# Kernel optimization log

Measured on AMD Instinct MI355X. Metric: run time of the kernel, lower is better.

Reference implementation:

```python
import jax, jax.numpy as jnp
import numpy as np

HEADS = 8
DIM_KEY = 64
DIM_VALUE = 192
DIM = 1536
NRPF = 192  # num_rel_pos_features, divisible by 6
SEQ = DIM_VALUE * HEADS  # 1536; source code reshapes with n = dim_value*heads as seq len
BATCH = 4


def get_positional_embed(seq_len, feature_size):
    # distances: (2*seq_len - 1,)
    distances = jnp.arange(-seq_len + 1, seq_len, dtype=jnp.float32)
    absd = jnp.abs(distances)[:, None]
    nb = feature_size // 6  # num_basis_per_class (3 fns * 2 for sign)
    # exponential
    max_range = np.log(seq_len) / np.log(2.0)
    half_life = 2.0 ** jnp.linspace(3.0, max_range, nb)
    pe_exp = jnp.exp(-jnp.log(2.0) / half_life[None, :] * absd)
    # central mask
    center_widths = 2.0 ** jnp.arange(1, nb + 1, dtype=jnp.float32) - 1.0
    pe_cm = (center_widths[None, :] > absd).astype(jnp.float32)
    # gamma
    stddev = seq_len / (2.0 * nb)
    start_mean = seq_len / nb
    mean = jnp.linspace(start_mean, float(seq_len), nb)[None, :]
    concentration = (mean / stddev) ** 2
    rate = mean / (stddev ** 2)
    log_unnorm = jax.scipy.special.xlogy(concentration - 1.0, absd) - rate * absd
    log_norm = jax.scipy.special.gammaln(concentration) - concentration * jnp.log(rate)
    probs = jnp.exp(log_unnorm - log_norm) + 1e-8
    pe_g = probs / jnp.max(probs, axis=-1, keepdims=True)
    emb = jnp.concatenate([pe_exp, pe_cm, pe_g], axis=-1)  # (2n-1, feature_size/2)
    return jnp.concatenate([emb, jnp.sign(distances)[:, None] * emb], axis=-1)


def relative_shift(x):
    # x: (b, h, t1, t2) with t2 = 2*t1 - 1 -> (b, h, t1, t1)
    b, h, t1, t2 = x.shape
    x = jnp.pad(x, ((0, 0), (0, 0), (0, 0), (1, 0)))  # (b,h,t1,t2+1)
    x = x.reshape(b, h, t2 + 1, t1)[:, :, 1:, :].reshape(b, h, t1, t2)
    return x[..., : (t2 + 2) // 2]


def setup_inputs() -> dict:
    key = jax.random.key(0)
    ks = jax.random.split(key, 9)
    s = 0.02
    return {
        "x": jax.random.normal(ks[0], (BATCH, SEQ, DIM), jnp.float32),
        "Wq": jax.random.normal(ks[1], (DIM, DIM_KEY * HEADS), jnp.float32) * s,
        "Wk": jax.random.normal(ks[2], (DIM, DIM_KEY * HEADS), jnp.float32) * s,
        "Wv": jax.random.normal(ks[3], (DIM, DIM_VALUE * HEADS), jnp.float32) * s,
        "Wrel": jax.random.normal(ks[4], (NRPF, DIM_KEY * HEADS), jnp.float32) * s,
        "rel_content_bias": jax.random.normal(ks[5], (1, HEADS, 1, DIM_KEY), jnp.float32),
        "rel_pos_bias": jax.random.normal(ks[6], (1, HEADS, 1, DIM_KEY), jnp.float32),
        "Wout": jax.random.normal(ks[7], (DIM_VALUE * HEADS, DIM), jnp.float32) * s,
        "b_out": jnp.zeros((DIM,), jnp.float32),
    }


def reference(x, Wq, Wk, Wv, Wrel, rel_content_bias, rel_pos_bias, Wout, b_out):
    b, n, _ = x.shape
    h, dk, dv = HEADS, DIM_KEY, DIM_VALUE
    scale = dk ** -0.5
    q = (x @ Wq).reshape(b, n, h, dk).transpose(0, 2, 1, 3) * scale  # (b,h,n,dk)
    k = (x @ Wk).reshape(b, n, h, dk).transpose(0, 2, 1, 3)
    v = (x @ Wv).reshape(b, n, h, dv).transpose(0, 2, 1, 3)
    content_logits = jnp.einsum('bhid,bhjd->bhij', q + rel_content_bias, k)
    positions = get_positional_embed(n, NRPF)  # (2n-1, NRPF)
    rel_k = (positions @ Wrel).reshape(2 * n - 1, h, dk).transpose(1, 0, 2)  # (h,2n-1,dk)
    rel_logits = jnp.einsum('bhid,hjd->bhij', q + rel_pos_bias, rel_k)  # (b,h,n,2n-1)
    rel_logits = relative_shift(rel_logits)  # (b,h,n,n)
    attn = jax.nn.softmax(content_logits + rel_logits, axis=-1)
    out = jnp.einsum('bhij,bhjd->bhid', attn, v)  # (b,h,n,dv)
    out = out.transpose(0, 2, 1, 3).reshape(b, n, h * dv)
    return out @ Wout + b_out
```

## Files before the change

kernel.cpp:

```cpp
#include <hip/hip_runtime.h>
#include <cmath>

#define B_SZ    4
#define N_SEQ   1536
#define D_MODEL 1536
#define H_N     8
#define DK      64
#define DV      192
#define HDK     512
#define HDV     1536
#define NRPF    192
#define NB      32
#define NREL    3071
#define QKS     2560
#define SM_BASE 12.0f

typedef unsigned short u16;
typedef __attribute__((ext_vector_type(8))) short short8;
typedef __attribute__((ext_vector_type(4))) float f32x4;

#define MFMA_B16(a, b, c) __builtin_amdgcn_mfma_f32_16x16x32_bf16(a, b, c, 0, 0, 0)

__device__ __forceinline__ float bf2f(u16 u) {
    union { unsigned u; float f; } x; x.u = ((unsigned)u) << 16; return x.f;
}
__device__ __forceinline__ u16 f2bf(float f) {
    union { float f; unsigned u; } x; x.f = f;
    unsigned r = x.u + 0x7FFFu + ((x.u >> 16) & 1u);
    return (u16)(r >> 16);
}
__device__ __forceinline__ void gload16(const u16* g, u16* l) {
    __builtin_amdgcn_global_load_lds(
        (const __attribute__((address_space(1))) unsigned int*)(const void*)g,
        (__attribute__((address_space(3))) unsigned int*)(void*)l, 16, 0, 0);
}

__global__ __launch_bounds__(256) void prep_kernel(
    const float* __restrict__ x,
    const float* __restrict__ Wq, const float* __restrict__ Wk,
    const float* __restrict__ Wv, const float* __restrict__ Wout,
    const float* __restrict__ Wrel,
    u16* __restrict__ posb, u16* __restrict__ xb,
    u16* __restrict__ wqkvt, u16* __restrict__ woutt, u16* __restrict__ wrelt) {
    const int z = blockIdx.z;
    const int tid = threadIdx.x;
    if (z < 5) {
        const float* W; u16* Wt; int K, N; float scale = 1.0f;
        if (z == 0)      { W = Wq;   Wt = wqkvt;                        K = 1536; N = 512;  scale = 0.125f; }
        else if (z == 1) { W = Wk;   Wt = wqkvt + (size_t)512 * 1536;   K = 1536; N = 512;  }
        else if (z == 2) { W = Wv;   Wt = wqkvt + (size_t)1024 * 1536;  K = 1536; N = 1536; }
        else if (z == 3) { W = Wout; Wt = woutt;                        K = 1536; N = 1536; }
        else             { W = Wrel; Wt = wrelt;                        K = 192;  N = 512;  }
        __shared__ float tile[32][33];
        int n0 = blockIdx.x * 32, k0 = blockIdx.y * 32;
        if (n0 >= N || k0 >= K) return;
        int tx = tid & 31, ty = tid >> 5;
        for (int r = ty; r < 32; r += 8) tile[r][tx] = W[(size_t)(k0 + r) * N + n0 + tx];
        __syncthreads();
        for (int r = ty; r < 32; r += 8)
            Wt[(size_t)(n0 + r) * K + k0 + tx] = f2bf(tile[tx][r] * scale);
    } else if (z == 5) {
        const int r = blockIdx.y * 64 + blockIdx.x;
        const int j = tid;
        if (r >= NREL) {
            if (j < 96) {
                posb[(size_t)r * NRPF + j] = 0;
                posb[(size_t)r * NRPF + 96 + j] = 0;
            }
            return;
        }
        __shared__ float gprobs[NB];
        float dist = (float)(r - (N_SEQ - 1));
        float absd = fabsf(dist);
        int cls = j >> 5, jj = j & 31;
        float val = 0.0f;
        if (j < 96) {
            if (cls == 0) {
                const float max_range = 10.584962500721156f;
                float hl = exp2f(3.0f + (float)jj * (max_range - 3.0f) / 31.0f);
                val = expf(-0.6931471805599453f / hl * absd);
            } else if (cls == 1) {
                float cw = exp2f((float)(jj + 1)) - 1.0f;
                val = (cw > absd) ? 1.0f : 0.0f;
            } else {
                float mean = 48.0f + (float)jj * (1536.0f - 48.0f) / 31.0f;
                float conc = (mean / 24.0f) * (mean / 24.0f);
                float rate = mean / 576.0f;
                float lu = (conc - 1.0f) * logf(absd) - rate * absd;
                float ln = lgammaf(conc) - conc * logf(rate);
                float prob = expf(lu - ln) + 1e-8f;
                gprobs[jj] = prob;
                val = prob;
            }
        }
        __syncthreads();
        if (j < 96) {
            if (cls == 2) {
                float mx = gprobs[0];
                #pragma unroll
                for (int t = 1; t < NB; ++t) mx = fmaxf(mx, gprobs[t]);
                val = val / mx;
            }
            float sgn = (dist > 0.f) ? 1.f : ((dist < 0.f) ? -1.f : 0.f);
            posb[(size_t)r * NRPF + j]      = f2bf(val);
            posb[(size_t)r * NRPF + 96 + j] = f2bf(sgn * val);
        }
    } else {
        const int n8 = (B_SZ * N_SEQ) * D_MODEL / 8;
        const float4* p = (const float4*)x;
        for (int i = (blockIdx.y * 64 + blockIdx.x) * 256 + tid; i < n8; i += 64 * 48 * 256) {
            float4 a = p[i * 2], bq = p[i * 2 + 1];
            short8 o;
            o[0] = (short)f2bf(a.x);  o[1] = (short)f2bf(a.y);
            o[2] = (short)f2bf(a.z);  o[3] = (short)f2bf(a.w);
            o[4] = (short)f2bf(bq.x); o[5] = (short)f2bf(bq.y);
            o[6] = (short)f2bf(bq.z); o[7] = (short)f2bf(bq.w);
            *(short8*)(xb + (size_t)i * 8) = o;
        }
    }
}

#define BM 128
#define BN 128
#define BK 64
__device__ __forceinline__ void gemm_body(
    const u16* __restrict__ A, const u16* __restrict__ Bt,
    u16* __restrict__ Cb, float* __restrict__ Cf,
    const float* __restrict__ bias, int Mstore, int N, int K) {
    __shared__ u16 sA[BM * BK] __attribute__((aligned(16)));
    __shared__ u16 sB[BN * BK] __attribute__((aligned(16)));
    const int tid  = threadIdx.x;
    const int lane = tid & 63;
    const int w    = tid >> 6;
    const int wm   = w >> 1, wn = w & 1;
    const int row0 = blockIdx.y * BM, col0 = blockIdx.x * BN;

    f32x4 acc[4][4];
    #pragma unroll
    for (int i = 0; i < 4; ++i)
        #pragma unroll
        for (int j = 0; j < 4; ++j) acc[i][j] = (f32x4){0.f, 0.f, 0.f, 0.f};

    int srow[4], soff[4];
    #pragma unroll
    for (int i = 0; i < 4; ++i) {
        const int ci = i * 256 + tid;
        const int r  = ci >> 3;
        const int lc = (ci & 7) ^ (r & 7);
        srow[i] = r;
        soff[i] = lc * 8;
    }

    for (int kt = 0; kt < K; kt += BK) {
        #pragma unroll
        for (int i = 0; i < 4; ++i) {
            gload16(A + (size_t)(row0 + srow[i]) * K + kt + soff[i],
                    sA + (i * 256 + w * 64) * 8);
            gload16(Bt + (size_t)(col0 + srow[i]) * K + kt + soff[i],
                    sB + (i * 256 + w * 64) * 8);
        }
        __syncthreads();
        short8 af[2][4], bg[2][4];
        #pragma unroll
        for (int s = 0; s < 2; ++s) {
            #pragma unroll
            for (int mi = 0; mi < 4; ++mi) {
                const int rr = wm * 64 + mi * 16 + (lane & 15);
                af[s][mi] = *(const short8*)&sA[rr * 64 + (((s * 4 + (lane >> 4)) ^ (rr & 7)) * 8)];
            }
            #pragma unroll
            for (int ni = 0; ni < 4; ++ni) {
                const int rr = wn * 64 + ni * 16 + (lane & 15);
                bg[s][ni] = *(const short8*)&sB[rr * 64 + (((s * 4 + (lane >> 4)) ^ (rr & 7)) * 8)];
            }
        }
        #pragma unroll
        for (int s = 0; s < 2; ++s)
            #pragma unroll
            for (int mi = 0; mi < 4; ++mi)
                #pragma unroll
                for (int ni = 0; ni < 4; ++ni)
                    acc[mi][ni] = MFMA_B16(af[s][mi], bg[s][ni], acc[mi][ni]);
        __syncthreads();
    }
    const int rb = (lane >> 4) * 4;
    const int cl = lane & 15;
    #pragma unroll
    for (int mi = 0; mi < 4; ++mi) {
        #pragma unroll
        for (int r = 0; r < 4; ++r) {
            const int gr = row0 + wm * 64 + mi * 16 + rb + r;
            if (gr >= Mstore) continue;
            #pragma unroll
            for (int ni = 0; ni < 4; ++ni) {
                const int gc = col0 + wn * 64 + ni * 16 + cl;
                float v = acc[mi][ni][r];
                if (bias) v += bias[gc];
                if (Cb) Cb[(size_t)gr * N + gc] = f2bf(v);
                else    Cf[(size_t)gr * N + gc] = v;
            }
        }
    }
}

__global__ __launch_bounds__(256) void gemm_bf16(
    const u16* __restrict__ A, const u16* __restrict__ Bt,
    u16* __restrict__ Cb, float* __restrict__ Cf,
    const float* __restrict__ bias, int Mstore, int N, int K) {
    gemm_body(A, Bt, Cb, Cf, bias, Mstore, N, K);
}

__global__ __launch_bounds__(256) void gemm_qkv_rel(
    const u16* __restrict__ xb, const u16* __restrict__ wqkvt, u16* __restrict__ qkvb,
    const u16* __restrict__ posb, const u16* __restrict__ wrelt, u16* __restrict__ relkb) {
    if (blockIdx.z == 0) {
        gemm_body(xb, wqkvt, qkvb, nullptr, nullptr, B_SZ * N_SEQ, QKS, D_MODEL);
    } else {
        if (blockIdx.y * BM >= 3072 || blockIdx.x * BN >= HDK) return;
        gemm_body(posb, wrelt, relkb, nullptr, nullptr, 3072, HDK, NRPF);
    }
}

__global__ __launch_bounds__(256) void transpose_v(const u16* __restrict__ qkv,
                                                   u16* __restrict__ vt) {
    __shared__ u16 tile[64][72];
    int nt = blockIdx.x, ct = blockIdx.y, bh = blockIdx.z;
    int b = bh >> 3, h = bh & 7;
    int tid = threadIdx.x;
    for (int t = tid; t < 512; t += 256) {
        int r = t >> 3, ch = t & 7;
        short8 v = *(const short8*)(qkv + ((size_t)(b * N_SEQ + nt * 64 + r)) * QKS
                                        + 1024 + h * DV + ct * 64 + ch * 8);
        #pragma unroll
        for (int e = 0; e < 8; ++e) tile[ch * 8 + e][r] = (u16)v[e];
    }
    __syncthreads();
    for (int t = tid; t < 512; t += 256) {
        int c = t >> 3, ch = t & 7;
        short8 v;
        #pragma unroll
        for (int e = 0; e < 8; ++e) v[e] = (short)tile[c][ch * 8 + e];
        *(short8*)(vt + ((size_t)((b * 8 + h) * DV + ct * 64 + c)) * N_SEQ
                      + nt * 64 + ch * 8) = v;
    }
}

__global__ __launch_bounds__(256, 3) void attn_mfma(
    const u16* __restrict__ qb, const u16* __restrict__ kb,
    const u16* __restrict__ vtb, const u16* __restrict__ relkb,
    const float* __restrict__ cbias, const float* __restrict__ pbias,
    u16* __restrict__ att) {
    __shared__ u16 sK[2 * 64 * 64] __attribute__((aligned(16)));
    __shared__ u16 sP[64 * 64] __attribute__((aligned(16)));
    __shared__ u16 sRW[192 * 64] __attribute__((aligned(16)));
    __shared__ float sL[64];

    const int tid  = threadIdx.x;
    const int lane = tid & 63;
    const int w    = tid >> 6;
    const int h    = blockIdx.x & 7;
    const int q9   = blockIdx.x >> 3;
    const int b    = q9 / 24;
    const int i0   = (q9 % 24) * 64;
    const int rbase0 = (N_SEQ - 64) - i0;

    const int c15 = lane & 15;
    const int g   = lane >> 4;
    const int g4  = g << 2;
    const int arow = w * 16 + c15;
    const int growb = w * 16 + g4;

    for (int t = tid; t < 512; t += 256) {
        const int row = t >> 3, ch = t & 7;
        short8 v = *(const short8*)(qb + ((size_t)(b * N_SEQ + i0 + row)) * QKS
                                       + h * DK + ch * 8);
        short8 c8, p8;
        #pragma unroll
        for (int e = 0; e < 8; ++e) {
            float f = bf2f((u16)v[e]);
            c8[e] = (short)f2bf(f + cbias[h * DK + ch * 8 + e]);
            p8[e] = (short)f2bf(f + pbias[h * DK + ch * 8 + e]);
        }
        const int dst = row * 64 + ((ch ^ (row & 7)) * 8);
        *(short8*)&sK[dst] = c8;
        *(short8*)&sP[dst] = p8;
    }
    __syncthreads();

    short8 aqc[2], aqp[2];
    #pragma unroll
    for (int s = 0; s < 2; ++s) {
        const int off = arow * 64 + (((s * 4 + g) ^ (arow & 7)) * 8);
        aqc[s] = *(const short8*)&sK[off];
        aqp[s] = *(const short8*)&sP[off];
    }
    __syncthreads();

    auto stage_k = [&](int j0s, int buf) {
        #pragma unroll
        for (int i = 0; i < 2; ++i) {
            const int ci = i * 256 + tid, row = ci >> 3;
            const int sch = ((ci & 7) ^ (row & 7)) * 8;
            gload16(kb + ((size_t)(b * N_SEQ + j0s + row)) * QKS + h * DK + sch,
                    sK + buf * 4096 + ci * 8);
        }
    };
    auto stage_r = [&](int lr0) {
        const int pw0 = lr0 % 192;
        #pragma unroll
        for (int i = 0; i < 2; ++i) {
            const int ci = i * 256 + tid, row = ci >> 3;
            const int sch = ((ci & 7) ^ ((pw0 + row) & 7)) * 8;
            gload16(relkb + ((size_t)(rbase0 + lr0 + row)) * HDK + h * DK + sch,
                    sRW + pw0 * 64 + ci * 8);
        }
    };

    stage_k(0, 0);
    stage_r(0);
    stage_r(64);
    asm volatile("s_waitcnt vmcnt(0) lgkmcnt(0)" ::: "memory");
    __builtin_amdgcn_sched_barrier(0);
    __builtin_amdgcn_s_barrier();

    f32x4 O[12];
    #pragma unroll
    for (int i = 0; i < 12; ++i) O[i] = (f32x4){0.f, 0.f, 0.f, 0.f};
    float L[4] = {0.f, 0.f, 0.f, 0.f};

    for (int jt = 0; jt < 24; ++jt) {
        const int j0 = jt * 64;
        if (jt < 23) {
            stage_k(j0 + 64, (jt + 1) & 1);
            stage_r(j0 + 128);
        }
        f32x4 S[4], G5[5];
        #pragma unroll
        for (int f = 0; f < 4; ++f) S[f] = (f32x4){0.f, 0.f, 0.f, 0.f};
        #pragma unroll
        for (int t = 0; t < 5; ++t) G5[t] = (f32x4){0.f, 0.f, 0.f, 0.f};
        const int kbase = (jt & 1) * 4096;
        const int ph = (jt % 3) * 64;
        #pragma unroll
        for (int s = 0; s < 2; ++s) {
            short8 kf[4], rf[5];
            #pragma unroll
            for (int f = 0; f < 4; ++f) {
                const int br = f * 16 + c15;
                kf[f] = *(const short8*)&sK[kbase + br * 64 + (((s * 4 + g) ^ (br & 7)) * 8)];
            }
            #pragma unroll
            for (int t = 0; t < 5; ++t) {
                int lrb = ph + (3 - w + t) * 16;
                if (lrb >= 192) lrb -= 192;
                const int pr = lrb + c15;
                rf[t] = *(const short8*)&sRW[pr * 64 + (((s * 4 + g) ^ (pr & 7)) * 8)];
            }
            #pragma unroll
            for (int f = 0; f < 4; ++f) S[f] = MFMA_B16(aqc[s], kf[f], S[f]);
            #pragma unroll
            for (int t = 0; t < 5; ++t) G5[t] = MFMA_B16(aqp[s], rf[t], G5[t]);
        }
        #pragma unroll
        for (int r = 0; r < 4; ++r) {
            const int src = (lane & 48) | ((c15 + 15 - g4 - r) & 15);
            const float rot0 = __shfl(G5[0][r], src, 64);
            const float rot1 = __shfl(G5[1][r], src, 64);
            const float rot2 = __shfl(G5[2][r], src, 64);
            const float rot3 = __shfl(G5[3][r], src, 64);
            const float rot4 = __shfl(G5[4][r], src, 64);
            const bool wrap = (c15 - g4) > r;
            S[0][r] += wrap ? rot1 : rot0;
            S[1][r] += wrap ? rot2 : rot1;
            S[2][r] += wrap ? rot3 : rot2;
            S[3][r] += wrap ? rot4 : rot3;
        }
        #pragma unroll
        for (int r = 0; r < 4; ++r) {
            #pragma unroll
            for (int f = 0; f < 4; ++f) {
                const float pe = __expf(S[f][r] - SM_BASE);
                S[f][r] = pe;
                L[r] += pe;
            }
        }
        #pragma unroll
        for (int f = 0; f < 4; ++f) {
            const int jj = f * 16 + c15;
            #pragma unroll
            for (int r = 0; r < 4; ++r) {
                const int ii = growb + r;
                sP[ii * 64 + (((jj >> 3) ^ (ii & 7)) * 8) + (jj & 7)] = f2bf(S[f][r]);
            }
        }
        asm volatile("s_waitcnt lgkmcnt(0)" ::: "memory");
        __builtin_amdgcn_sched_barrier(0);
        __builtin_amdgcn_s_barrier();
        #pragma unroll
        for (int s = 0; s < 2; ++s) {
            const u16* vp = vtb + ((size_t)((b * 8 + h) * DV + w * 48 + c15)) * N_SEQ
                                + j0 + s * 32 + 8 * g;
            short8 vf[3];
            #pragma unroll
            for (int cf3 = 0; cf3 < 3; ++cf3)
                vf[cf3] = *(const short8*)(vp + (size_t)cf3 * 16 * N_SEQ);
            #pragma unroll
            for (int rfi = 0; rfi < 4; ++rfi) {
                const int prow = rfi * 16 + c15;
                short8 a = *(const short8*)&sP[prow * 64 + (((s * 4 + g) ^ (prow & 7)) * 8)];
                #pragma unroll
                for (int cf3 = 0; cf3 < 3; ++cf3)
                    O[rfi * 3 + cf3] = MFMA_B16(a, vf[cf3], O[rfi * 3 + cf3]);
            }
        }
        asm volatile("s_waitcnt vmcnt(0) lgkmcnt(0)" ::: "memory");
        __builtin_amdgcn_sched_barrier(0);
        __builtin_amdgcn_s_barrier();
    }
    #pragma unroll
    for (int r = 0; r < 4; ++r) {
        float l = L[r];
        l += __shfl_xor(l, 1, 64);
        l += __shfl_xor(l, 2, 64);
        l += __shfl_xor(l, 4, 64);
        l += __shfl_xor(l, 8, 64);
        L[r] = l;
    }
    if (c15 == 0) {
        #pragma unroll
        for (int r = 0; r < 4; ++r) sL[growb + r] = L[r];
    }
    __syncthreads();
    #pragma unroll
    for (int rfi = 0; rfi < 4; ++rfi) {
        #pragma unroll
        for (int r = 0; r < 4; ++r) {
            const int row = rfi * 16 + g4 + r;
            const float inv = 1.0f / sL[row];
            #pragma unroll
            for (int cf3 = 0; cf3 < 3; ++cf3) {
                att[((size_t)(b * N_SEQ + i0 + row)) * HDV + h * DV
                    + w * 48 + cf3 * 16 + c15] = f2bf(O[rfi * 3 + cf3][r] * inv);
            }
        }
    }
}

extern "C" void kernel_launch(void* const* d_in, const int* in_sizes, int n_in,
                              void* d_out, int out_size, void* d_ws, size_t ws_size,
                              hipStream_t stream) {
    const float* x    = (const float*)d_in[0];
    const float* Wq   = (const float*)d_in[1];
    const float* Wk   = (const float*)d_in[2];
    const float* Wv   = (const float*)d_in[3];
    const float* Wrel = (const float*)d_in[4];
    const float* cb   = (const float*)d_in[5];
    const float* pb   = (const float*)d_in[6];
    const float* Wout = (const float*)d_in[7];
    const float* bout = (const float*)d_in[8];
    float* out = (float*)d_out;

    const int M = B_SZ * N_SEQ;
    u16* ws16  = (u16*)d_ws;
    u16* xb    = ws16;
    u16* qkvb  = xb    + (size_t)M * HDV;
    u16* vtb   = qkvb  + (size_t)M * QKS;
    u16* posb  = vtb   + (size_t)M * HDV;
    u16* relkb = posb  + (size_t)3072 * NRPF;
    u16* wqkvt = relkb + (size_t)3072 * HDK;
    u16* woutt = wqkvt + (size_t)QKS * D_MODEL;
    u16* wrelt = woutt + (size_t)D_MODEL * HDV;
    u16* attb  = xb;

    dim3 blk(256);
    prep_kernel<<<dim3(64, 48, 7), blk, 0, stream>>>(
        x, Wq, Wk, Wv, Wout, Wrel, posb, xb, wqkvt, woutt, wrelt);
    gemm_qkv_rel<<<dim3(QKS / BN, M / BM, 2), blk, 0, stream>>>(
        xb, wqkvt, qkvb, posb, wrelt, relkb);
    transpose_v<<<dim3(N_SEQ / 64, DV / 64, B_SZ * H_N), blk, 0, stream>>>(qkvb, vtb);
    attn_mfma<<<768, blk, 0, stream>>>(
        qkvb, qkvb + 512, vtb, relkb, cb, pb, attb);
    gemm_bf16<<<dim3(D_MODEL / BN, M / BM), blk, 0, stream>>>(
        attb, woutt, nullptr, out, bout, M, D_MODEL, HDV);
}
```

Measured before the change: 266.0 us.

## Shrink attention LDS buffers and raise occupancy to four blocks per CU

Drops the K double buffer and cuts the relative-key ring from three to two 64-row windows, using XOR addressing instead of a modulo-three phase. This lowers LDS per block so launch bounds can ask for four resident blocks instead of three. Prefetch of the next K and rel-key tiles now starts after the softmax barrier and overlaps only the PV product, not the QK phase, so there is less latency hiding inside a block in exchange for more blocks per CU. The higher launch bound also tightens the register budget, which may cause spills.

Measured after the change: 389.8 us. 1.47x slower.

```diff
diff --git a/kernel.cpp b/kernel.cpp
--- a/kernel.cpp
+++ b/kernel.cpp
@@ -245,14 +245,14 @@
     }
 }
 
-__global__ __launch_bounds__(256, 3) void attn_mfma(
+__global__ __launch_bounds__(256, 4) void attn_mfma(
     const u16* __restrict__ qb, const u16* __restrict__ kb,
     const u16* __restrict__ vtb, const u16* __restrict__ relkb,
     const float* __restrict__ cbias, const float* __restrict__ pbias,
     u16* __restrict__ att) {
-    __shared__ u16 sK[2 * 64 * 64] __attribute__((aligned(16)));
+    __shared__ u16 sK[64 * 64] __attribute__((aligned(16)));
     __shared__ u16 sP[64 * 64] __attribute__((aligned(16)));
-    __shared__ u16 sRW[192 * 64] __attribute__((aligned(16)));
+    __shared__ u16 sRW[128 * 64] __attribute__((aligned(16)));
     __shared__ float sL[64];
 
     const int tid  = threadIdx.x;
@@ -296,32 +296,29 @@
     }
     __syncthreads();
 
-    auto stage_k = [&](int j0s, int buf) {
+    auto stage_k = [&](int j0s) {
         #pragma unroll
         for (int i = 0; i < 2; ++i) {
             const int ci = i * 256 + tid, row = ci >> 3;
             const int sch = ((ci & 7) ^ (row & 7)) * 8;
             gload16(kb + ((size_t)(b * N_SEQ + j0s + row)) * QKS + h * DK + sch,
-                    sK + buf * 4096 + ci * 8);
+                    sK + ci * 8);
         }
     };
-    auto stage_r = [&](int lr0) {
-        const int pw0 = lr0 % 192;
+    auto stage_r = [&](int gr0, int pw0) {
         #pragma unroll
         for (int i = 0; i < 2; ++i) {
             const int ci = i * 256 + tid, row = ci >> 3;
-            const int sch = ((ci & 7) ^ ((pw0 + row) & 7)) * 8;
-            gload16(relkb + ((size_t)(rbase0 + lr0 + row)) * HDK + h * DK + sch,
+            const int sch = ((ci & 7) ^ (row & 7)) * 8;
+            gload16(relkb + ((size_t)(rbase0 + gr0 + row)) * HDK + h * DK + sch,
                     sRW + pw0 * 64 + ci * 8);
         }
     };
 
-    stage_k(0, 0);
-    stage_r(0);
-    stage_r(64);
-    asm volatile("s_waitcnt vmcnt(0) lgkmcnt(0)" ::: "memory");
-    __builtin_amdgcn_sched_barrier(0);
-    __builtin_amdgcn_s_barrier();
+    stage_k(0);
+    stage_r(0, 0);
+    stage_r(64, 64);
+    __syncthreads();
 
     f32x4 O[12];
     #pragma unroll
@@ -330,30 +327,24 @@
 
     for (int jt = 0; jt < 24; ++jt) {
         const int j0 = jt * 64;
-        if (jt < 23) {
-            stage_k(j0 + 64, (jt + 1) & 1);
-            stage_r(j0 + 128);
-        }
+        const int poff = (jt & 1) << 6;
         f32x4 S[4], G5[5];
         #pragma unroll
         for (int f = 0; f < 4; ++f) S[f] = (f32x4){0.f, 0.f, 0.f, 0.f};
         #pragma unroll
         for (int t = 0; t < 5; ++t) G5[t] = (f32x4){0.f, 0.f, 0.f, 0.f};
-        const int kbase = (jt & 1) * 4096;
-        const int ph = (jt % 3) * 64;
         #pragma unroll
         for (int s = 0; s < 2; ++s) {
             short8 kf[4], rf[5];
             #pragma unroll
             for (int f = 0; f < 4; ++f) {
                 const int br = f * 16 + c15;
-                kf[f] = *(const short8*)&sK[kbase + br * 64 + (((s * 4 + g) ^ (br & 7)) * 8)];
+                kf[f] = *(const short8*)&sK[br * 64 + (((s * 4 + g) ^ (br & 7)) * 8)];
             }
             #pragma unroll
             for (int t = 0; t < 5; ++t) {
-                int lrb = ph + (3 - w + t) * 16;
-                if (lrb >= 192) lrb -= 192;
-                const int pr = lrb + c15;
+                const int lr = (3 - w + t) * 16 + c15;
+                const int pr = lr ^ poff;
                 rf[t] = *(const short8*)&sRW[pr * 64 + (((s * 4 + g) ^ (pr & 7)) * 8)];
             }
             #pragma unroll
@@ -393,9 +384,11 @@
                 sP[ii * 64 + (((jj >> 3) ^ (ii & 7)) * 8) + (jj & 7)] = f2bf(S[f][r]);
             }
         }
-        asm volatile("s_waitcnt lgkmcnt(0)" ::: "memory");
-        __builtin_amdgcn_sched_barrier(0);
-        __builtin_amdgcn_s_barrier();
+        __syncthreads();
+        if (jt < 23) {
+            stage_k(j0 + 64);
+            stage_r(j0 + 128, poff);
+        }
         #pragma unroll
         for (int s = 0; s < 2; ++s) {
             const u16* vp = vtb + ((size_t)((b * 8 + h) * DV + w * 48 + c15)) * N_SEQ
@@ -413,9 +406,7 @@
                     O[rfi * 3 + cf3] = MFMA_B16(a, vf[cf3], O[rfi * 3 + cf3]);
             }
         }
-        asm volatile("s_waitcnt vmcnt(0) lgkmcnt(0)" ::: "memory");
-        __builtin_amdgcn_sched_barrier(0);
-        __builtin_amdgcn_s_barrier();
+        __syncthreads();
     }
     #pragma unroll
     for (int r = 0; r < 4; ++r) {
```
